# Optimization experiments

Measured on AMD Instinct MI355X. Metric: run time of the kernel, lower is better.

## Reference

```python
import jax, jax.numpy as jnp
import numpy as np

P = 4            # capsule pose side
D = P * P        # capsule dim = 16
N_CLASSES = 10
N_ROUT = 3


def squash(s, axis=-1):
    sq = (s ** 2).sum(axis=axis, keepdims=True)
    scale = sq / (1.0 + sq)
    return scale * s / jnp.sqrt(sq)


def setup_inputs() -> dict:
    key = jax.random.key(0)
    k1, k2, k3 = jax.random.split(key, 3)
    N, C, W, H = 32, 32, 16, 16
    l = jax.random.normal(k1, (N, C, D, W, H), dtype=jnp.float32)
    g = jax.random.normal(k2, (N, N_CLASSES, D), dtype=jnp.float32)
    weight = jax.random.normal(k3, (1, C, 1, N_CLASSES, P, P), dtype=jnp.float32)
    return {"l": l, "g": g, "weight": weight}


def reference(l, g, weight):
    N, C, Dd, W, H = l.shape
    K = N_CLASSES
    # (N, C, D, W, H) -> (N, C, W*H, P, P)
    lr = jnp.transpose(l, (0, 1, 3, 4, 2)).reshape(N, C, W * H, P, P)
    w = weight.reshape(C, K, P, P)
    # votes: broadcasted small matmul over (N, C, WH, K)
    V = jnp.einsum('ncwij,ckjl->ncwkil', lr, w)          # (N, C, WH, K, P, P)
    V = V.reshape(N, 1, 1, C * W * H, K, Dd)             # (N,1,1,B,K,D)
    gb = g[:, None, None, None, :, :]                    # (N,1,1,1,K,D)
    b = (gb * V).sum(axis=-1, keepdims=True)             # (N,1,1,B,K,1)
    # dynamic routing, iters = N_ROUT
    for i in range(N_ROUT):
        c = jax.nn.softmax(b, axis=4)
        v = squash((c * V).sum(axis=3, keepdims=True))   # (N,1,1,1,K,D)
        if i != N_ROUT - 1:
            b = b + (V * v).sum(axis=-1, keepdims=True)
    a = jax.nn.sigmoid(jnp.linalg.norm(v, axis=-1))      # (N,1,1,1,K)
    v = v.reshape(N, K, Dd)
    a = a.reshape(N, K)
    return (a, v)
```

## Files before the change

kernel.cpp:

```cpp
#include <hip/hip_runtime.h>
#include <math.h>

#define NB 32
#define CB 32
#define KC 10
#define PAD_LRT 260
#define PAD_TP  168

__global__ __launch_bounds__(256) void caps_main(
    const float* __restrict__ l,
    const float* __restrict__ g,
    const float* __restrict__ weight,
    const float* __restrict__ sp0,
    const float* __restrict__ sp1,
    float* __restrict__ s_out,
    int nv)
{
    __shared__ __align__(16) float w_lds[160];
    __shared__ __align__(16) float aeff_lds[160];
    __shared__ __align__(16) float E_lds[160];
    __shared__ __align__(16) float lrT[16 * PAD_LRT];
    __shared__ __align__(16) float c_lds[KC * 256];
    __shared__ __align__(16) float Tp[16 * PAD_TP];
    __shared__ __align__(16) float T_lds[160];

    const int tid = threadIdx.x;
    const int n = blockIdx.x >> 5;
    const int c = blockIdx.x & 31;

    if (tid < 160) w_lds[tid] = weight[c * 160 + tid];

    float lr[16];
    const float* lbase = l + (size_t)(n * CB + c) * 4096 + tid;
    #pragma unroll
    for (int ij = 0; ij < 16; ++ij) lr[ij] = lbase[ij * 256];
    #pragma unroll
    for (int ij = 0; ij < 16; ++ij) lrT[ij * PAD_LRT + tid] = lr[ij];

    if (tid < 160) {
        float a = g[n * 160 + tid];
        if (nv > 0) {
            const float* sp = sp0 + (size_t)n * (CB * 160) + tid;
            float t0 = 0.f, t1 = 0.f, t2 = 0.f, t3 = 0.f;
            #pragma unroll
            for (int cc = 0; cc < 32; cc += 4) {
                t0 += sp[cc * 160];       t1 += sp[(cc + 1) * 160];
                t2 += sp[(cc + 2) * 160]; t3 += sp[(cc + 3) * 160];
            }
            float ssum = (t0 + t1) + (t2 + t3);
            float sq = ssum * ssum;
            sq += __shfl_xor(sq, 1, 16);
            sq += __shfl_xor(sq, 2, 16);
            sq += __shfl_xor(sq, 4, 16);
            sq += __shfl_xor(sq, 8, 16);
            sq = fmaxf(sq, 1e-30f);
            a += ssum * sq / ((1.f + sq) * sqrtf(sq));
        }
        if (nv > 1) {
            const float* sp = sp1 + (size_t)n * (CB * 160) + tid;
            float t0 = 0.f, t1 = 0.f, t2 = 0.f, t3 = 0.f;
            #pragma unroll
            for (int cc = 0; cc < 32; cc += 4) {
                t0 += sp[cc * 160];       t1 += sp[(cc + 1) * 160];
                t2 += sp[(cc + 2) * 160]; t3 += sp[(cc + 3) * 160];
            }
            float ssum = (t0 + t1) + (t2 + t3);
            float sq = ssum * ssum;
            sq += __shfl_xor(sq, 1, 16);
            sq += __shfl_xor(sq, 2, 16);
            sq += __shfl_xor(sq, 4, 16);
            sq += __shfl_xor(sq, 8, 16);
            sq = fmaxf(sq, 1e-30f);
            a += ssum * sq / ((1.f + sq) * sqrtf(sq));
        }
        aeff_lds[tid] = a;
    }
    __syncthreads();

    if (tid < 160) {
        const int k = tid >> 4;
        const int i = (tid >> 2) & 3;
        const int j = tid & 3;
        const float* av = aeff_lds + k * 16;
        const float* wk = w_lds + k * 16;
        float e = 0.f;
        #pragma unroll
        for (int ll = 0; ll < 4; ++ll)
            e = fmaf(av[i * 4 + ll], wk[j * 4 + ll], e);
        E_lds[tid] = e;
    }
    __syncthreads();

    float b[KC];
    #pragma unroll
    for (int k = 0; k < KC; ++k) {
        const float4* e4 = (const float4*)(E_lds + k * 16);
        float4 e0 = e4[0], e1 = e4[1], e2 = e4[2], e3 = e4[3];
        float acc = 0.f;
        acc = fmaf(lr[0], e0.x, acc);  acc = fmaf(lr[1], e0.y, acc);
        acc = fmaf(lr[2], e0.z, acc);  acc = fmaf(lr[3], e0.w, acc);
        acc = fmaf(lr[4], e1.x, acc);  acc = fmaf(lr[5], e1.y, acc);
        acc = fmaf(lr[6], e1.z, acc);  acc = fmaf(lr[7], e1.w, acc);
        acc = fmaf(lr[8], e2.x, acc);  acc = fmaf(lr[9], e2.y, acc);
        acc = fmaf(lr[10], e2.z, acc); acc = fmaf(lr[11], e2.w, acc);
        acc = fmaf(lr[12], e3.x, acc); acc = fmaf(lr[13], e3.y, acc);
        acc = fmaf(lr[14], e3.z, acc); acc = fmaf(lr[15], e3.w, acc);
        b[k] = acc;
    }
    float mx = b[0];
    #pragma unroll
    for (int k = 1; k < KC; ++k) mx = fmaxf(mx, b[k]);
    float sum = 0.f;
    #pragma unroll
    for (int k = 0; k < KC; ++k) { b[k] = __expf(b[k] - mx); sum += b[k]; }
    const float inv = 1.f / sum;
    #pragma unroll
    for (int k = 0; k < KC; ++k) c_lds[k * 256 + tid] = b[k] * inv;
    __syncthreads();

    {
        const int ij = tid & 15;
        const int mg = tid >> 4;
        const float4* lp = (const float4*)(lrT + ij * PAD_LRT + mg * 16);
        float4 l0 = lp[0], l1 = lp[1], l2 = lp[2], l3 = lp[3];
        #pragma unroll
        for (int k = 0; k < KC; ++k) {
            const float4* cp = (const float4*)(c_lds + k * 256 + mg * 16);
            float4 c0 = cp[0], c1 = cp[1], c2 = cp[2], c3 = cp[3];
            float t = 0.f;
            t = fmaf(c0.x, l0.x, t); t = fmaf(c0.y, l0.y, t);
            t = fmaf(c0.z, l0.z, t); t = fmaf(c0.w, l0.w, t);
            t = fmaf(c1.x, l1.x, t); t = fmaf(c1.y, l1.y, t);
            t = fmaf(c1.z, l1.z, t); t = fmaf(c1.w, l1.w, t);
            t = fmaf(c2.x, l2.x, t); t = fmaf(c2.y, l2.y, t);
            t = fmaf(c2.z, l2.z, t); t = fmaf(c2.w, l2.w, t);
            t = fmaf(c3.x, l3.x, t); t = fmaf(c3.y, l3.y, t);
            t = fmaf(c3.z, l3.z, t); t = fmaf(c3.w, l3.w, t);
            Tp[mg * PAD_TP + k * 16 + ij] = t;
        }
    }
    __syncthreads();

    if (tid < 160) {
        float t = 0.f;
        #pragma unroll
        for (int mg2 = 0; mg2 < 16; ++mg2) t += Tp[mg2 * PAD_TP + tid];
        T_lds[tid] = t;
    }
    __syncthreads();

    if (tid < 160) {
        const int k = tid >> 4;
        const int i = (tid >> 2) & 3;
        const int le = tid & 3;
        float sv = 0.f;
        #pragma unroll
        for (int j = 0; j < 4; ++j)
            sv = fmaf(T_lds[k * 16 + i * 4 + j], w_lds[k * 16 + j * 4 + le], sv);
        s_out[(size_t)blockIdx.x * 160 + tid] = sv;
    }
}

__global__ __launch_bounds__(256) void caps_final(
    const float* __restrict__ sp2, float* __restrict__ out)
{
    const int idx = blockIdx.x * 256 + threadIdx.x;
    const int nk = idx >> 4;
    const int d = idx & 15;
    const int n = nk / 10;
    const int k = nk - n * 10;
    const float* sp = sp2 + (size_t)n * (CB * 160) + k * 16 + d;
    float t0 = 0.f, t1 = 0.f, t2 = 0.f, t3 = 0.f;
    #pragma unroll
    for (int cc = 0; cc < 32; cc += 4) {
        t0 += sp[cc * 160];       t1 += sp[(cc + 1) * 160];
        t2 += sp[(cc + 2) * 160]; t3 += sp[(cc + 3) * 160];
    }
    float ssum = (t0 + t1) + (t2 + t3);
    float sq = ssum * ssum;
    sq += __shfl_xor(sq, 1, 16);
    sq += __shfl_xor(sq, 2, 16);
    sq += __shfl_xor(sq, 4, 16);
    sq += __shfl_xor(sq, 8, 16);
    sq = fmaxf(sq, 1e-30f);
    out[320 + nk * 16 + d] = ssum * sq / ((1.f + sq) * sqrtf(sq));
    if (d == 0) {
        const float nrm = sq / (1.f + sq);
        out[nk] = 1.f / (1.f + __expf(-nrm));
    }
}

extern "C" void kernel_launch(void* const* d_in, const int* in_sizes, int n_in,
                              void* d_out, int out_size, void* d_ws, size_t ws_size,
                              hipStream_t stream) {
    const float* l = (const float*)d_in[0];
    const float* g = (const float*)d_in[1];
    const float* w = (const float*)d_in[2];
    float* out = (float*)d_out;
    float* ws = (float*)d_ws;

    float* s0 = ws;
    float* s1 = ws + 163840;
    float* s2 = ws + 327680;

    caps_main<<<dim3(NB * CB), dim3(256), 0, stream>>>(l, g, w, nullptr, nullptr, s0, 0);
    caps_main<<<dim3(NB * CB), dim3(256), 0, stream>>>(l, g, w, s0, nullptr, s1, 1);
    caps_main<<<dim3(NB * CB), dim3(256), 0, stream>>>(l, g, w, s0, s1, s2, 2);
    caps_final<<<dim3(20), dim3(256), 0, stream>>>(s2, out);
}
```

Measured before the change: 29.03 us.

## Fuse routing iterations into one cooperative kernel with grid sync

Replaces the three routing launches and the final launch with one cooperative kernel of 512 blocks. Each block handles two capsule channels, keeps their inputs in registers and LDS across all three iterations, and uses grid.sync between iterations. This removes repeated kernel launch overhead and re-reading of the input tensor each iteration, at the cost of grid-wide barriers, lower parallelism per block, and higher register and LDS pressure. Host-side occupancy queries run on every call, and the original multi-launch path is kept as a fallback.

```diff
diff --git a/kernel.cpp b/kernel.cpp
--- a/kernel.cpp
+++ b/kernel.cpp
@@ -1,5 +1,8 @@
 #include <hip/hip_runtime.h>
+#include <hip/hip_cooperative_groups.h>
 #include <math.h>
+
+namespace cg = cooperative_groups;
 
 #define NB 32
 #define CB 32
@@ -7,94 +10,30 @@
 #define PAD_LRT 260
 #define PAD_TP  168
 
-__global__ __launch_bounds__(256) void caps_main(
-    const float* __restrict__ l,
-    const float* __restrict__ g,
-    const float* __restrict__ weight,
-    const float* __restrict__ sp0,
-    const float* __restrict__ sp1,
-    float* __restrict__ s_out,
-    int nv)
-{
-    __shared__ __align__(16) float w_lds[160];
-    __shared__ __align__(16) float aeff_lds[160];
-    __shared__ __align__(16) float E_lds[160];
-    __shared__ __align__(16) float lrT[16 * PAD_LRT];
-    __shared__ __align__(16) float c_lds[KC * 256];
-    __shared__ __align__(16) float Tp[16 * PAD_TP];
-    __shared__ __align__(16) float T_lds[160];
-
-    const int tid = threadIdx.x;
-    const int n = blockIdx.x >> 5;
-    const int c = blockIdx.x & 31;
-
-    if (tid < 160) w_lds[tid] = weight[c * 160 + tid];
-
-    float lr[16];
-    const float* lbase = l + (size_t)(n * CB + c) * 4096 + tid;
-    #pragma unroll
-    for (int ij = 0; ij < 16; ++ij) lr[ij] = lbase[ij * 256];
-    #pragma unroll
-    for (int ij = 0; ij < 16; ++ij) lrT[ij * PAD_LRT + tid] = lr[ij];
-
-    if (tid < 160) {
-        float a = g[n * 160 + tid];
-        if (nv > 0) {
-            const float* sp = sp0 + (size_t)n * (CB * 160) + tid;
-            float t0 = 0.f, t1 = 0.f, t2 = 0.f, t3 = 0.f;
-            #pragma unroll
-            for (int cc = 0; cc < 32; cc += 4) {
-                t0 += sp[cc * 160];       t1 += sp[(cc + 1) * 160];
-                t2 += sp[(cc + 2) * 160]; t3 += sp[(cc + 3) * 160];
-            }
-            float ssum = (t0 + t1) + (t2 + t3);
-            float sq = ssum * ssum;
-            sq += __shfl_xor(sq, 1, 16);
-            sq += __shfl_xor(sq, 2, 16);
-            sq += __shfl_xor(sq, 4, 16);
-            sq += __shfl_xor(sq, 8, 16);
-            sq = fmaxf(sq, 1e-30f);
-            a += ssum * sq / ((1.f + sq) * sqrtf(sq));
-        }
-        if (nv > 1) {
-            const float* sp = sp1 + (size_t)n * (CB * 160) + tid;
-            float t0 = 0.f, t1 = 0.f, t2 = 0.f, t3 = 0.f;
-            #pragma unroll
-            for (int cc = 0; cc < 32; cc += 4) {
-                t0 += sp[cc * 160];       t1 += sp[(cc + 1) * 160];
-                t2 += sp[(cc + 2) * 160]; t3 += sp[(cc + 3) * 160];
-            }
-            float ssum = (t0 + t1) + (t2 + t3);
-            float sq = ssum * ssum;
-            sq += __shfl_xor(sq, 1, 16);
-            sq += __shfl_xor(sq, 2, 16);
-            sq += __shfl_xor(sq, 4, 16);
-            sq += __shfl_xor(sq, 8, 16);
-            sq = fmaxf(sq, 1e-30f);
-            a += ssum * sq / ((1.f + sq) * sqrtf(sq));
-        }
-        aeff_lds[tid] = a;
-    }
-    __syncthreads();
-
-    if (tid < 160) {
-        const int k = tid >> 4;
-        const int i = (tid >> 2) & 3;
-        const int j = tid & 3;
-        const float* av = aeff_lds + k * 16;
-        const float* wk = w_lds + k * 16;
-        float e = 0.f;
-        #pragma unroll
-        for (int ll = 0; ll < 4; ++ll)
-            e = fmaf(av[i * 4 + ll], wk[j * 4 + ll], e);
-        E_lds[tid] = e;
-    }
-    __syncthreads();
-
+__device__ __forceinline__ float squash_term(const float* __restrict__ sp, int n, int tid) {
+    const float* p = sp + (size_t)n * (CB * 160) + tid;
+    float t0 = 0.f, t1 = 0.f, t2 = 0.f, t3 = 0.f;
+    #pragma unroll
+    for (int cc = 0; cc < 32; cc += 4) {
+        t0 += p[cc * 160];       t1 += p[(cc + 1) * 160];
+        t2 += p[(cc + 2) * 160]; t3 += p[(cc + 3) * 160];
+    }
+    float ssum = (t0 + t1) + (t2 + t3);
+    float sq = ssum * ssum;
+    sq += __shfl_xor(sq, 1, 16);
+    sq += __shfl_xor(sq, 2, 16);
+    sq += __shfl_xor(sq, 4, 16);
+    sq += __shfl_xor(sq, 8, 16);
+    sq = fmaxf(sq, 1e-30f);
+    return ssum * sq / ((1.f + sq) * sqrtf(sq));
+}
+
+__device__ __forceinline__ void softmax_c(const float lr[16], const float* __restrict__ E,
+                                          float* __restrict__ c_out, int tid) {
     float b[KC];
     #pragma unroll
     for (int k = 0; k < KC; ++k) {
-        const float4* e4 = (const float4*)(E_lds + k * 16);
+        const float4* e4 = (const float4*)(E + k * 16);
         float4 e0 = e4[0], e1 = e4[1], e2 = e4[2], e3 = e4[3];
         float acc = 0.f;
         acc = fmaf(lr[0], e0.x, acc);  acc = fmaf(lr[1], e0.y, acc);
@@ -115,40 +54,46 @@
     for (int k = 0; k < KC; ++k) { b[k] = __expf(b[k] - mx); sum += b[k]; }
     const float inv = 1.f / sum;
     #pragma unroll
-    for (int k = 0; k < KC; ++k) c_lds[k * 256 + tid] = b[k] * inv;
-    __syncthreads();
-
-    {
-        const int ij = tid & 15;
-        const int mg = tid >> 4;
-        const float4* lp = (const float4*)(lrT + ij * PAD_LRT + mg * 16);
-        float4 l0 = lp[0], l1 = lp[1], l2 = lp[2], l3 = lp[3];
-        #pragma unroll
-        for (int k = 0; k < KC; ++k) {
-            const float4* cp = (const float4*)(c_lds + k * 256 + mg * 16);
-            float4 c0 = cp[0], c1 = cp[1], c2 = cp[2], c3 = cp[3];
-            float t = 0.f;
-            t = fmaf(c0.x, l0.x, t); t = fmaf(c0.y, l0.y, t);
-            t = fmaf(c0.z, l0.z, t); t = fmaf(c0.w, l0.w, t);
-            t = fmaf(c1.x, l1.x, t); t = fmaf(c1.y, l1.y, t);
-            t = fmaf(c1.z, l1.z, t); t = fmaf(c1.w, l1.w, t);
-            t = fmaf(c2.x, l2.x, t); t = fmaf(c2.y, l2.y, t);
-            t = fmaf(c2.z, l2.z, t); t = fmaf(c2.w, l2.w, t);
-            t = fmaf(c3.x, l3.x, t); t = fmaf(c3.y, l3.y, t);
-            t = fmaf(c3.z, l3.z, t); t = fmaf(c3.w, l3.w, t);
-            Tp[mg * PAD_TP + k * 16 + ij] = t;
-        }
-    }
-    __syncthreads();
-
-    if (tid < 160) {
+    for (int k = 0; k < KC; ++k) c_out[k * 256 + tid] = b[k] * inv;
+}
+
+__device__ __forceinline__ void tp_stage(const float* __restrict__ lrTp,
+                                         const float* __restrict__ cl,
+                                         float* __restrict__ Tp, int tid) {
+    const int ij = tid & 15;
+    const int mg = tid >> 4;
+    const float4* lp = (const float4*)(lrTp + ij * PAD_LRT + mg * 16);
+    float4 l0 = lp[0], l1 = lp[1], l2 = lp[2], l3 = lp[3];
+    #pragma unroll
+    for (int k = 0; k < KC; ++k) {
+        const float4* cp = (const float4*)(cl + k * 256 + mg * 16);
+        float4 c0 = cp[0], c1 = cp[1], c2 = cp[2], c3 = cp[3];
         float t = 0.f;
-        #pragma unroll
-        for (int mg2 = 0; mg2 < 16; ++mg2) t += Tp[mg2 * PAD_TP + tid];
-        T_lds[tid] = t;
-    }
-    __syncthreads();
-
+        t = fmaf(c0.x, l0.x, t); t = fmaf(c0.y, l0.y, t);
+        t = fmaf(c0.z, l0.z, t); t = fmaf(c0.w, l0.w, t);
+        t = fmaf(c1.x, l1.x, t); t = fmaf(c1.y, l1.y, t);
+        t = fmaf(c1.z, l1.z, t); t = fmaf(c1.w, l1.w, t);
+        t = fmaf(c2.x, l2.x, t); t = fmaf(c2.y, l2.y, t);
+        t = fmaf(c2.z, l2.z, t); t = fmaf(c2.w, l2.w, t);
+        t = fmaf(c3.x, l3.x, t); t = fmaf(c3.y, l3.y, t);
+        t = fmaf(c3.z, l3.z, t); t = fmaf(c3.w, l3.w, t);
+        Tp[mg * PAD_TP + k * 16 + ij] = t;
+    }
+}
+
+__device__ __forceinline__ void t_reduce(const float* __restrict__ Tp,
+                                         float* __restrict__ T, int tid) {
+    if (tid < 160) {
+        float t = 0.f;
+        #pragma unroll
+        for (int mg = 0; mg < 16; ++mg) t += Tp[mg * PAD_TP + tid];
+        T[tid] = t;
+    }
+}
+
+__device__ __forceinline__ void s_write(const float* __restrict__ T,
+                                        const float* __restrict__ w,
+                                        float* __restrict__ s_base, int tid) {
     if (tid < 160) {
         const int k = tid >> 4;
         const int i = (tid >> 2) & 3;
@@ -156,9 +101,178 @@
         float sv = 0.f;
         #pragma unroll
         for (int j = 0; j < 4; ++j)
-            sv = fmaf(T_lds[k * 16 + i * 4 + j], w_lds[k * 16 + j * 4 + le], sv);
-        s_out[(size_t)blockIdx.x * 160 + tid] = sv;
-    }
+            sv = fmaf(T[k * 16 + i * 4 + j], w[k * 16 + j * 4 + le], sv);
+        s_base[tid] = sv;
+    }
+}
+
+__global__ __launch_bounds__(256, 2) void caps_fused(
+    const float* __restrict__ l,
+    const float* __restrict__ g,
+    const float* __restrict__ weight,
+    float* __restrict__ s0,
+    float* __restrict__ s1,
+    float* __restrict__ s2,
+    float* __restrict__ out)
+{
+    __shared__ __align__(16) float w_lds[2][160];
+    __shared__ __align__(16) float aeff_lds[160];
+    __shared__ __align__(16) float E_lds[2][160];
+    __shared__ __align__(16) float lrT[2][16 * PAD_LRT];
+    __shared__ __align__(16) float c_lds[KC * 256];
+    __shared__ __align__(16) float Tp[16 * PAD_TP];
+    __shared__ __align__(16) float T_lds[2][160];
+
+    cg::grid_group grid = cg::this_grid();
+    const int tid = threadIdx.x;
+    const int bid = blockIdx.x;
+    const int n  = bid >> 4;
+    const int c0 = bid & 15;
+    const int c1 = c0 + 16;
+
+    if (tid < 160) {
+        w_lds[0][tid] = weight[c0 * 160 + tid];
+        w_lds[1][tid] = weight[c1 * 160 + tid];
+    }
+
+    float lrA[16], lrB[16];
+    {
+        const float* la = l + (size_t)(n * CB + c0) * 4096 + tid;
+        const float* lb = l + (size_t)(n * CB + c1) * 4096 + tid;
+        #pragma unroll
+        for (int ij = 0; ij < 16; ++ij) { lrA[ij] = la[ij * 256]; lrT[0][ij * PAD_LRT + tid] = lrA[ij]; }
+        #pragma unroll
+        for (int ij = 0; ij < 16; ++ij) { lrB[ij] = lb[ij * 256]; lrT[1][ij * PAD_LRT + tid] = lrB[ij]; }
+    }
+
+    #pragma unroll 1
+    for (int it = 0; it < 3; ++it) {
+        const float* sp0 = (it >= 1) ? s0 : nullptr;
+        const float* sp1 = (it >= 2) ? s1 : nullptr;
+        float* s_out = (it == 0) ? s0 : (it == 1) ? s1 : s2;
+
+        if (tid < 160) {
+            float a = g[n * 160 + tid];
+            if (sp0) a += squash_term(sp0, n, tid);
+            if (sp1) a += squash_term(sp1, n, tid);
+            aeff_lds[tid] = a;
+        }
+        __syncthreads();
+
+        if (tid < 160) {
+            const int k = tid >> 4, i = (tid >> 2) & 3, j = tid & 3;
+            const float* av = aeff_lds + k * 16;
+            float e0 = 0.f, e1 = 0.f;
+            #pragma unroll
+            for (int ll = 0; ll < 4; ++ll) {
+                const float a = av[i * 4 + ll];
+                e0 = fmaf(a, w_lds[0][k * 16 + j * 4 + ll], e0);
+                e1 = fmaf(a, w_lds[1][k * 16 + j * 4 + ll], e1);
+            }
+            E_lds[0][tid] = e0;
+            E_lds[1][tid] = e1;
+        }
+        __syncthreads();
+
+        softmax_c(lrA, E_lds[0], c_lds, tid);
+        __syncthreads();
+        tp_stage(lrT[0], c_lds, Tp, tid);
+        __syncthreads();
+        t_reduce(Tp, T_lds[0], tid);
+        softmax_c(lrB, E_lds[1], c_lds, tid);
+        __syncthreads();
+        tp_stage(lrT[1], c_lds, Tp, tid);
+        s_write(T_lds[0], w_lds[0], s_out + (size_t)(n * CB + c0) * 160, tid);
+        __syncthreads();
+        t_reduce(Tp, T_lds[1], tid);
+        __syncthreads();
+        s_write(T_lds[1], w_lds[1], s_out + (size_t)(n * CB + c1) * 160, tid);
+
+        grid.sync();
+    }
+
+    if (bid < 20) {
+        const int idx = bid * 256 + tid;
+        const int nk = idx >> 4;
+        const int d = idx & 15;
+        const int nn = nk / 10;
+        const int k = nk - nn * 10;
+        const float* sp = s2 + (size_t)nn * (CB * 160) + k * 16 + d;
+        float t0 = 0.f, t1 = 0.f, t2 = 0.f, t3 = 0.f;
+        #pragma unroll
+        for (int cc = 0; cc < 32; cc += 4) {
+            t0 += sp[cc * 160];       t1 += sp[(cc + 1) * 160];
+            t2 += sp[(cc + 2) * 160]; t3 += sp[(cc + 3) * 160];
+        }
+        float ssum = (t0 + t1) + (t2 + t3);
+        float sq = ssum * ssum;
+        sq += __shfl_xor(sq, 1, 16);
+        sq += __shfl_xor(sq, 2, 16);
+        sq += __shfl_xor(sq, 4, 16);
+        sq += __shfl_xor(sq, 8, 16);
+        sq = fmaxf(sq, 1e-30f);
+        out[320 + nk * 16 + d] = ssum * sq / ((1.f + sq) * sqrtf(sq));
+        if (d == 0) {
+            const float nrm = sq / (1.f + sq);
+            out[nk] = 1.f / (1.f + __expf(-nrm));
+        }
+    }
+}
+
+__global__ __launch_bounds__(256) void caps_main(
+    const float* __restrict__ l, const float* __restrict__ g,
+    const float* __restrict__ weight,
+    const float* __restrict__ sp0, const float* __restrict__ sp1,
+    float* __restrict__ s_out, int nv)
+{
+    __shared__ __align__(16) float w_lds[160];
+    __shared__ __align__(16) float aeff_lds[160];
+    __shared__ __align__(16) float E_lds[160];
+    __shared__ __align__(16) float lrT1[16 * PAD_LRT];
+    __shared__ __align__(16) float c_lds[KC * 256];
+    __shared__ __align__(16) float Tp[16 * PAD_TP];
+    __shared__ __align__(16) float T_lds[160];
+
+    const int tid = threadIdx.x;
+    const int n = blockIdx.x >> 5;
+    const int c = blockIdx.x & 31;
+
+    if (tid < 160) w_lds[tid] = weight[c * 160 + tid];
+
+    float lr[16];
+    const float* lbase = l + (size_t)(n * CB + c) * 4096 + tid;
+    #pragma unroll
+    for (int ij = 0; ij < 16; ++ij) lr[ij] = lbase[ij * 256];
+    #pragma unroll
+    for (int ij = 0; ij < 16; ++ij) lrT1[ij * PAD_LRT + tid] = lr[ij];
+
+    if (tid < 160) {
+        float a = g[n * 160 + tid];
+        if (nv > 0) a += squash_term(sp0, n, tid);
+        if (nv > 1) a += squash_term(sp1, n, tid);
+        aeff_lds[tid] = a;
+    }
+    __syncthreads();
+
+    if (tid < 160) {
+        const int k = tid >> 4, i = (tid >> 2) & 3, j = tid & 3;
+        const float* av = aeff_lds + k * 16;
+        const float* wk = w_lds + k * 16;
+        float e = 0.f;
+        #pragma unroll
+        for (int ll = 0; ll < 4; ++ll)
+            e = fmaf(av[i * 4 + ll], wk[j * 4 + ll], e);
+        E_lds[tid] = e;
+    }
+    __syncthreads();
+
+    softmax_c(lr, E_lds, c_lds, tid);
+    __syncthreads();
+    tp_stage(lrT1, c_lds, Tp, tid);
+    __syncthreads();
+    t_reduce(Tp, T_lds, tid);
+    __syncthreads();
+    s_write(T_lds, w_lds, s_out + (size_t)blockIdx.x * 160, tid);
 }
 
 __global__ __launch_bounds__(256) void caps_final(
@@ -203,8 +317,22 @@
     float* s1 = ws + 163840;
     float* s2 = ws + 327680;
 
-    caps_main<<<dim3(NB * CB), dim3(256), 0, stream>>>(l, g, w, nullptr, nullptr, s0, 0);
-    caps_main<<<dim3(NB * CB), dim3(256), 0, stream>>>(l, g, w, s0, nullptr, s1, 1);
-    caps_main<<<dim3(NB * CB), dim3(256), 0, stream>>>(l, g, w, s0, s1, s2, 2);
-    caps_final<<<dim3(20), dim3(256), 0, stream>>>(s2, out);
-}
+    int perCU = 0, nCU = 0, dev = 0;
+    (void)hipGetDevice(&dev);
+    (void)hipDeviceGetAttribute(&nCU, hipDeviceAttributeMultiprocessorCount, dev);
+    (void)hipOccupancyMaxActiveBlocksPerMultiprocessor(&perCU, caps_fused, 256, 0);
+
+    hipError_t e = hipErrorUnknown;
+    if ((long)perCU * (long)nCU >= 512) {
+        void* args[] = { (void*)&l, (void*)&g, (void*)&w,
+                         (void*)&s0, (void*)&s1, (void*)&s2, (void*)&out };
+        e = hipLaunchCooperativeKernel((void*)caps_fused, dim3(512), dim3(256),
+                                       args, 0, stream);
+    }
+    if (e != hipSuccess) {
+        caps_main<<<dim3(NB * CB), dim3(256), 0, stream>>>(l, g, w, nullptr, nullptr, s0, 0);
+        caps_main<<<dim3(NB * CB), dim3(256), 0, stream>>>(l, g, w, s0, nullptr, s1, 1);
+        caps_main<<<dim3(NB * CB), dim3(256), 0, stream>>>(l, g, w, s0, s1, s2, 2);
+        caps_final<<<dim3(20), dim3(256), 0, stream>>>(s2, out);
+    }
+}
```

Result: no change. 29.39 us (+1.2%).

## Transpose partial-s layout to c-contiguous and vectorize reductions; split Tp stage per thread

Applied to the files above, without the earlier changes.

Partial s results are now stored with the channel index innermost, so each reducing thread reads its 32 partials as eight contiguous float4 loads instead of 32 strided scalar loads. The Tp stage is reorganized so each thread computes two ij outputs for five classes, reusing each loaded c vector across two accumulators. The layout change makes the per-block stores strided by 32 floats, which may hurt write coalescing.

```diff
diff --git a/kernel.cpp b/kernel.cpp
--- a/kernel.cpp
+++ b/kernel.cpp
@@ -7,94 +7,30 @@
 #define PAD_LRT 260
 #define PAD_TP  168
 
-__global__ __launch_bounds__(256) void caps_main(
-    const float* __restrict__ l,
-    const float* __restrict__ g,
-    const float* __restrict__ weight,
-    const float* __restrict__ sp0,
-    const float* __restrict__ sp1,
-    float* __restrict__ s_out,
-    int nv)
-{
-    __shared__ __align__(16) float w_lds[160];
-    __shared__ __align__(16) float aeff_lds[160];
-    __shared__ __align__(16) float E_lds[160];
-    __shared__ __align__(16) float lrT[16 * PAD_LRT];
-    __shared__ __align__(16) float c_lds[KC * 256];
-    __shared__ __align__(16) float Tp[16 * PAD_TP];
-    __shared__ __align__(16) float T_lds[160];
-
-    const int tid = threadIdx.x;
-    const int n = blockIdx.x >> 5;
-    const int c = blockIdx.x & 31;
-
-    if (tid < 160) w_lds[tid] = weight[c * 160 + tid];
-
-    float lr[16];
-    const float* lbase = l + (size_t)(n * CB + c) * 4096 + tid;
-    #pragma unroll
-    for (int ij = 0; ij < 16; ++ij) lr[ij] = lbase[ij * 256];
-    #pragma unroll
-    for (int ij = 0; ij < 16; ++ij) lrT[ij * PAD_LRT + tid] = lr[ij];
-
-    if (tid < 160) {
-        float a = g[n * 160 + tid];
-        if (nv > 0) {
-            const float* sp = sp0 + (size_t)n * (CB * 160) + tid;
-            float t0 = 0.f, t1 = 0.f, t2 = 0.f, t3 = 0.f;
-            #pragma unroll
-            for (int cc = 0; cc < 32; cc += 4) {
-                t0 += sp[cc * 160];       t1 += sp[(cc + 1) * 160];
-                t2 += sp[(cc + 2) * 160]; t3 += sp[(cc + 3) * 160];
-            }
-            float ssum = (t0 + t1) + (t2 + t3);
-            float sq = ssum * ssum;
-            sq += __shfl_xor(sq, 1, 16);
-            sq += __shfl_xor(sq, 2, 16);
-            sq += __shfl_xor(sq, 4, 16);
-            sq += __shfl_xor(sq, 8, 16);
-            sq = fmaxf(sq, 1e-30f);
-            a += ssum * sq / ((1.f + sq) * sqrtf(sq));
-        }
-        if (nv > 1) {
-            const float* sp = sp1 + (size_t)n * (CB * 160) + tid;
-            float t0 = 0.f, t1 = 0.f, t2 = 0.f, t3 = 0.f;
-            #pragma unroll
-            for (int cc = 0; cc < 32; cc += 4) {
-                t0 += sp[cc * 160];       t1 += sp[(cc + 1) * 160];
-                t2 += sp[(cc + 2) * 160]; t3 += sp[(cc + 3) * 160];
-            }
-            float ssum = (t0 + t1) + (t2 + t3);
-            float sq = ssum * ssum;
-            sq += __shfl_xor(sq, 1, 16);
-            sq += __shfl_xor(sq, 2, 16);
-            sq += __shfl_xor(sq, 4, 16);
-            sq += __shfl_xor(sq, 8, 16);
-            sq = fmaxf(sq, 1e-30f);
-            a += ssum * sq / ((1.f + sq) * sqrtf(sq));
-        }
-        aeff_lds[tid] = a;
-    }
-    __syncthreads();
-
-    if (tid < 160) {
-        const int k = tid >> 4;
-        const int i = (tid >> 2) & 3;
-        const int j = tid & 3;
-        const float* av = aeff_lds + k * 16;
-        const float* wk = w_lds + k * 16;
-        float e = 0.f;
-        #pragma unroll
-        for (int ll = 0; ll < 4; ++ll)
-            e = fmaf(av[i * 4 + ll], wk[j * 4 + ll], e);
-        E_lds[tid] = e;
-    }
-    __syncthreads();
-
+
+__device__ __forceinline__ float squash_term(const float* __restrict__ sp, int n, int tid) {
+    const float4* p = (const float4*)(sp + ((size_t)n * 160 + tid) * 32);
+    float4 q0 = p[0], q1 = p[1], q2 = p[2], q3 = p[3];
+    float4 q4 = p[4], q5 = p[5], q6 = p[6], q7 = p[7];
+    float ssum = (((q0.x + q0.y) + (q0.z + q0.w)) + ((q1.x + q1.y) + (q1.z + q1.w)))
+               + (((q2.x + q2.y) + (q2.z + q2.w)) + ((q3.x + q3.y) + (q3.z + q3.w)))
+               + (((q4.x + q4.y) + (q4.z + q4.w)) + ((q5.x + q5.y) + (q5.z + q5.w)))
+               + (((q6.x + q6.y) + (q6.z + q6.w)) + ((q7.x + q7.y) + (q7.z + q7.w)));
+    float sq = ssum * ssum;
+    sq += __shfl_xor(sq, 1, 16);
+    sq += __shfl_xor(sq, 2, 16);
+    sq += __shfl_xor(sq, 4, 16);
+    sq += __shfl_xor(sq, 8, 16);
+    sq = fmaxf(sq, 1e-30f);
+    return ssum * sq / ((1.f + sq) * sqrtf(sq));
+}
+
+__device__ __forceinline__ void softmax_c(const float lr[16], const float* __restrict__ E,
+                                          float* __restrict__ c_out, int tid) {
     float b[KC];
     #pragma unroll
     for (int k = 0; k < KC; ++k) {
-        const float4* e4 = (const float4*)(E_lds + k * 16);
+        const float4* e4 = (const float4*)(E + k * 16);
         float4 e0 = e4[0], e1 = e4[1], e2 = e4[2], e3 = e4[3];
         float acc = 0.f;
         acc = fmaf(lr[0], e0.x, acc);  acc = fmaf(lr[1], e0.y, acc);
@@ -115,40 +51,60 @@
     for (int k = 0; k < KC; ++k) { b[k] = __expf(b[k] - mx); sum += b[k]; }
     const float inv = 1.f / sum;
     #pragma unroll
-    for (int k = 0; k < KC; ++k) c_lds[k * 256 + tid] = b[k] * inv;
-    __syncthreads();
-
-    {
-        const int ij = tid & 15;
-        const int mg = tid >> 4;
-        const float4* lp = (const float4*)(lrT + ij * PAD_LRT + mg * 16);
-        float4 l0 = lp[0], l1 = lp[1], l2 = lp[2], l3 = lp[3];
-        #pragma unroll
-        for (int k = 0; k < KC; ++k) {
-            const float4* cp = (const float4*)(c_lds + k * 256 + mg * 16);
-            float4 c0 = cp[0], c1 = cp[1], c2 = cp[2], c3 = cp[3];
-            float t = 0.f;
-            t = fmaf(c0.x, l0.x, t); t = fmaf(c0.y, l0.y, t);
-            t = fmaf(c0.z, l0.z, t); t = fmaf(c0.w, l0.w, t);
-            t = fmaf(c1.x, l1.x, t); t = fmaf(c1.y, l1.y, t);
-            t = fmaf(c1.z, l1.z, t); t = fmaf(c1.w, l1.w, t);
-            t = fmaf(c2.x, l2.x, t); t = fmaf(c2.y, l2.y, t);
-            t = fmaf(c2.z, l2.z, t); t = fmaf(c2.w, l2.w, t);
-            t = fmaf(c3.x, l3.x, t); t = fmaf(c3.y, l3.y, t);
-            t = fmaf(c3.z, l3.z, t); t = fmaf(c3.w, l3.w, t);
-            Tp[mg * PAD_TP + k * 16 + ij] = t;
-        }
-    }
-    __syncthreads();
-
+    for (int k = 0; k < KC; ++k) c_out[k * 256 + tid] = b[k] * inv;
+}
+
+__device__ __forceinline__ void tp_stage(const float* __restrict__ lrTp,
+                                         const float* __restrict__ cl,
+                                         float* __restrict__ Tp, int tid) {
+    const int mg  = tid >> 4;
+    const int r   = tid & 15;
+    const int ij0 = (r & 7) * 2;
+    const int k0  = (r >> 3) * 5;
+    const float4* lp0 = (const float4*)(lrTp + ij0 * PAD_LRT + mg * 16);
+    const float4* lp1 = (const float4*)(lrTp + (ij0 + 1) * PAD_LRT + mg * 16);
+    float4 a0 = lp0[0], a1 = lp0[1], a2 = lp0[2], a3 = lp0[3];
+    float4 b0 = lp1[0], b1 = lp1[1], b2 = lp1[2], b3 = lp1[3];
+    #pragma unroll
+    for (int kk = 0; kk < 5; ++kk) {
+        const int k = k0 + kk;
+        const float4* cp = (const float4*)(cl + k * 256 + mg * 16);
+        float4 c0 = cp[0], c1 = cp[1], c2 = cp[2], c3 = cp[3];
+        float t0 = 0.f, t1 = 0.f;
+        t0 = fmaf(c0.x, a0.x, t0); t1 = fmaf(c0.x, b0.x, t1);
+        t0 = fmaf(c0.y, a0.y, t0); t1 = fmaf(c0.y, b0.y, t1);
+        t0 = fmaf(c0.z, a0.z, t0); t1 = fmaf(c0.z, b0.z, t1);
+        t0 = fmaf(c0.w, a0.w, t0); t1 = fmaf(c0.w, b0.w, t1);
+        t0 = fmaf(c1.x, a1.x, t0); t1 = fmaf(c1.x, b1.x, t1);
+        t0 = fmaf(c1.y, a1.y, t0); t1 = fmaf(c1.y, b1.y, t1);
+        t0 = fmaf(c1.z, a1.z, t0); t1 = fmaf(c1.z, b1.z, t1);
+        t0 = fmaf(c1.w, a1.w, t0); t1 = fmaf(c1.w, b1.w, t1);
+        t0 = fmaf(c2.x, a2.x, t0); t1 = fmaf(c2.x, b2.x, t1);
+        t0 = fmaf(c2.y, a2.y, t0); t1 = fmaf(c2.y, b2.y, t1);
+        t0 = fmaf(c2.z, a2.z, t0); t1 = fmaf(c2.z, b2.z, t1);
+        t0 = fmaf(c2.w, a2.w, t0); t1 = fmaf(c2.w, b2.w, t1);
+        t0 = fmaf(c3.x, a3.x, t0); t1 = fmaf(c3.x, b3.x, t1);
+        t0 = fmaf(c3.y, a3.y, t0); t1 = fmaf(c3.y, b3.y, t1);
+        t0 = fmaf(c3.z, a3.z, t0); t1 = fmaf(c3.z, b3.z, t1);
+        t0 = fmaf(c3.w, a3.w, t0); t1 = fmaf(c3.w, b3.w, t1);
+        Tp[mg * PAD_TP + k * 16 + ij0]     = t0;
+        Tp[mg * PAD_TP + k * 16 + ij0 + 1] = t1;
+    }
+}
+
+__device__ __forceinline__ void t_reduce(const float* __restrict__ Tp,
+                                         float* __restrict__ T, int tid) {
     if (tid < 160) {
         float t = 0.f;
         #pragma unroll
-        for (int mg2 = 0; mg2 < 16; ++mg2) t += Tp[mg2 * PAD_TP + tid];
-        T_lds[tid] = t;
-    }
-    __syncthreads();
-
+        for (int mg = 0; mg < 16; ++mg) t += Tp[mg * PAD_TP + tid];
+        T[tid] = t;
+    }
+}
+
+__device__ __forceinline__ void s_write(const float* __restrict__ T,
+                                        const float* __restrict__ w,
+                                        float* __restrict__ s, int n, int c, int tid) {
     if (tid < 160) {
         const int k = tid >> 4;
         const int i = (tid >> 2) & 3;
@@ -156,9 +112,65 @@
         float sv = 0.f;
         #pragma unroll
         for (int j = 0; j < 4; ++j)
-            sv = fmaf(T_lds[k * 16 + i * 4 + j], w_lds[k * 16 + j * 4 + le], sv);
-        s_out[(size_t)blockIdx.x * 160 + tid] = sv;
-    }
+            sv = fmaf(T[k * 16 + i * 4 + j], w[k * 16 + j * 4 + le], sv);
+        s[((size_t)n * 160 + tid) * 32 + c] = sv;
+    }
+}
+
+__global__ __launch_bounds__(256) void caps_main(
+    const float* __restrict__ l, const float* __restrict__ g,
+    const float* __restrict__ weight,
+    const float* __restrict__ sp0, const float* __restrict__ sp1,
+    float* __restrict__ s_out, int nv)
+{
+    __shared__ __align__(16) float w_lds[160];
+    __shared__ __align__(16) float aeff_lds[160];
+    __shared__ __align__(16) float E_lds[160];
+    __shared__ __align__(16) float lrT[16 * PAD_LRT];
+    __shared__ __align__(16) float c_lds[KC * 256];
+    __shared__ __align__(16) float Tp[16 * PAD_TP];
+    __shared__ __align__(16) float T_lds[160];
+
+    const int tid = threadIdx.x;
+    const int n = blockIdx.x >> 5;
+    const int c = blockIdx.x & 31;
+
+    if (tid < 160) w_lds[tid] = weight[c * 160 + tid];
+
+    float lr[16];
+    const float* lbase = l + (size_t)(n * CB + c) * 4096 + tid;
+    #pragma unroll
+    for (int ij = 0; ij < 16; ++ij) lr[ij] = lbase[ij * 256];
+    #pragma unroll
+    for (int ij = 0; ij < 16; ++ij) lrT[ij * PAD_LRT + tid] = lr[ij];
+
+    if (tid < 160) {
+        float a = g[n * 160 + tid];
+        if (nv > 0) a += squash_term(sp0, n, tid);
+        if (nv > 1) a += squash_term(sp1, n, tid);
+        aeff_lds[tid] = a;
+    }
+    __syncthreads();
+
+    if (tid < 160) {
+        const int k = tid >> 4, i = (tid >> 2) & 3, j = tid & 3;
+        const float* av = aeff_lds + k * 16;
+        const float* wk = w_lds + k * 16;
+        float e = 0.f;
+        #pragma unroll
+        for (int ll = 0; ll < 4; ++ll)
+            e = fmaf(av[i * 4 + ll], wk[j * 4 + ll], e);
+        E_lds[tid] = e;
+    }
+    __syncthreads();
+
+    softmax_c(lr, E_lds, c_lds, tid);
+    __syncthreads();
+    tp_stage(lrT, c_lds, Tp, tid);
+    __syncthreads();
+    t_reduce(Tp, T_lds, tid);
+    __syncthreads();
+    s_write(T_lds, w_lds, s_out, n, c, tid);
 }
 
 __global__ __launch_bounds__(256) void caps_final(
@@ -169,14 +181,13 @@
     const int d = idx & 15;
     const int n = nk / 10;
     const int k = nk - n * 10;
-    const float* sp = sp2 + (size_t)n * (CB * 160) + k * 16 + d;
-    float t0 = 0.f, t1 = 0.f, t2 = 0.f, t3 = 0.f;
-    #pragma unroll
-    for (int cc = 0; cc < 32; cc += 4) {
-        t0 += sp[cc * 160];       t1 += sp[(cc + 1) * 160];
-        t2 += sp[(cc + 2) * 160]; t3 += sp[(cc + 3) * 160];
-    }
-    float ssum = (t0 + t1) + (t2 + t3);
+    const float4* p = (const float4*)(sp2 + ((size_t)n * 160 + k * 16 + d) * 32);
+    float4 q0 = p[0], q1 = p[1], q2 = p[2], q3 = p[3];
+    float4 q4 = p[4], q5 = p[5], q6 = p[6], q7 = p[7];
+    float ssum = (((q0.x + q0.y) + (q0.z + q0.w)) + ((q1.x + q1.y) + (q1.z + q1.w)))
+               + (((q2.x + q2.y) + (q2.z + q2.w)) + ((q3.x + q3.y) + (q3.z + q3.w)))
+               + (((q4.x + q4.y) + (q4.z + q4.w)) + ((q5.x + q5.y) + (q5.z + q5.w)))
+               + (((q6.x + q6.y) + (q6.z + q6.w)) + ((q7.x + q7.y) + (q7.z + q7.w)));
     float sq = ssum * ssum;
     sq += __shfl_xor(sq, 1, 16);
     sq += __shfl_xor(sq, 2, 16);
```

After: 37.51 us. 29.2% more time.
